# Performance work log

Hardware: AMD Instinct MI355X
Metric: run time of the kernel (lower is better)

## Reference

```python
import jax, jax.numpy as jnp
import numpy as np
import math

NUM_HEADS = 12
EMBED_DIM = 768

def setup_inputs() -> dict:
    key = jax.random.key(0)
    ks = jax.random.split(key, 9)
    B, T, D = 2, 2048, EMBED_DIM
    s = 1.0 / math.sqrt(D)
    inp = {
        "x": jax.random.normal(ks[0], (B, T, D), dtype=jnp.float32),
        "Wq": jax.random.normal(ks[1], (D, D), dtype=jnp.float32) * s,
        "bq": jnp.zeros((D,), dtype=jnp.float32),
        "Wk": jax.random.normal(ks[2], (D, D), dtype=jnp.float32) * s,
        "bk": jnp.zeros((D,), dtype=jnp.float32),
        "Wv": jax.random.normal(ks[3], (D, D), dtype=jnp.float32) * s,
        "bv": jnp.zeros((D,), dtype=jnp.float32),
        "Wo": jax.random.normal(ks[4], (D, D), dtype=jnp.float32) * s,
        "bo": jnp.zeros((D,), dtype=jnp.float32),
    }
    return inp

def reference(x, Wq, bq, Wk, bk, Wv, bv, Wo, bo):
    B, T, D = x.shape
    H = NUM_HEADS
    Dh = D // H
    # QKV projections, split heads: [B, H, T, Dh]
    def proj(W, b):
        y = x @ W.T + b
        return y.reshape(B, T, H, Dh).transpose(0, 2, 1, 3)
    q = proj(Wq, bq)
    k = proj(Wk, bk)
    v = proj(Wv, bv)
    scores = jnp.einsum('bhtd,bhsd->bhts', q, k) / math.sqrt(Dh)  # [B,H,T,T]
    attn = jax.nn.softmax(scores, axis=-1)
    ctx = jnp.einsum('bhts,bhsd->bhtd', attn, v)  # [B,H,T,Dh]
    ctx = ctx.transpose(0, 2, 1, 3).reshape(B, T, D)
    out = ctx @ Wo.T + bo
    return out
```

## Files before the change

### kernel.cpp

```cpp
#include <hip/hip_runtime.h>
#include <math.h>

using f32x4   = __attribute__((ext_vector_type(4))) float;
using bf16x8  = __attribute__((ext_vector_type(8))) short;

constexpr int Bb = 2;
constexpr int T  = 2048;
constexpr int D  = 768;
constexpr int H  = 12;
constexpr int Dh = 64;
constexpr int M  = Bb * T;
constexpr int NQKV = 3 * D;
constexpr int NBH = Bb * H;
#define SCALE_Q 0.18033688011112042f

__device__ __forceinline__ unsigned short f2bf(float f) {
    unsigned u = __float_as_uint(f);
    u += 0x7fffu + ((u >> 16) & 1u);
    return (unsigned short)(u >> 16);
}

__device__ __forceinline__ ushort4 f2bf4(float4 f) {
    return make_ushort4(f2bf(f.x), f2bf(f.y), f2bf(f.z), f2bf(f.w));
}

__device__ __forceinline__ unsigned permpk(float hi_f, float lo_f) {
    return __builtin_amdgcn_perm(__float_as_uint(hi_f), __float_as_uint(lo_f),
                                 0x07060302u);
}

__device__ __forceinline__ void async_copy16(const void* g, void* lds_base) {
    __builtin_amdgcn_global_load_lds(
        (const __attribute__((address_space(1))) unsigned int*)g,
        (__attribute__((address_space(3))) unsigned int*)lds_base, 16, 0, 0);
}

__global__ __launch_bounds__(256) void prep_kernel(
    const float4* __restrict__ x,
    const float4* __restrict__ Wq, const float4* __restrict__ Wk,
    const float4* __restrict__ Wv, const float4* __restrict__ Wo,
    const float* __restrict__ bq, const float* __restrict__ bk, const float* __restrict__ bv,
    ushort4* __restrict__ Xb, ushort4* __restrict__ Wqkvb, ushort4* __restrict__ Wob,
    float* __restrict__ biasS)
{
    const int stride = gridDim.x * 256;
    const int i0 = blockIdx.x * 256 + threadIdx.x;
    const int NX = M * D / 4;
    const int NW = D * D / 4;
    for (int i = i0; i < NX; i += stride) Xb[i] = f2bf4(x[i]);
    for (int i = i0; i < NW; i += stride) {
        Wqkvb[i]          = f2bf4(Wq[i]);
        Wqkvb[NW + i]     = f2bf4(Wk[i]);
        Wqkvb[2 * NW + i] = f2bf4(Wv[i]);
        Wob[i]            = f2bf4(Wo[i]);
    }
    for (int i = i0; i < D; i += stride) {
        biasS[i]         = bq[i];
        biasS[D + i]     = bk[i];
        biasS[2 * D + i] = bv[i];
    }
}

template <int MODE, int TM, int DB>
__global__ __launch_bounds__(256) void gemm_bt_kernel(
    const unsigned short* __restrict__ A, const unsigned short* __restrict__ Bm,
    const float* __restrict__ bias, const int Kdim, const int Ndim,
    float* __restrict__ Cout,
    unsigned short* __restrict__ Qo, unsigned short* __restrict__ Ko,
    unsigned short* __restrict__ Vo)
{
    constexpr int IW  = TM / 32;
    constexpr int NCH = (TM + 128) / 8;
    constexpr int TB  = (TM + 128) * 128;
    __shared__ unsigned short Sm[(TM + 128) * 64 * (DB ? 2 : 1)];
    const int tid  = threadIdx.x;
    const int lane = tid & 63, wv = tid >> 6;
    const int l15  = lane & 15, l4 = lane >> 4;
    const int wr   = wv >> 1,  wc = wv & 1;

    const int lin = blockIdx.y * gridDim.x + blockIdx.x;
    const int gx  = (lin >> 3) % gridDim.x;
    const int gy  = (lin / (8 * gridDim.x)) * 8 + (lin & 7);
    const int row0 = gy * TM, col0 = gx * 128;

    auto stage = [&](int k0, int b) {
        #pragma unroll
        for (int ch0 = 0; ch0 < NCH; ch0 += 4) {
            const int ch = ch0 + wv;
            const int offb = ch * 1024;
            const int off  = offb + lane * 16;
            const int r  = off >> 7;
            const int bl = (off & 127) >> 4;
            const int gc = (bl ^ (r & 7)) << 3;
            const unsigned short* src = (r < TM)
                ? A  + (size_t)(row0 + r) * Kdim + k0 + gc
                : Bm + (size_t)(col0 + (r - TM)) * Kdim + k0 + gc;
            async_copy16(src, (char*)Sm + b * TB + offb);
        }
    };

    f32x4 acc[IW][4];
    #pragma unroll
    for (int i = 0; i < IW; ++i)
        #pragma unroll
        for (int j = 0; j < 4; ++j)
            acc[i][j] = (f32x4){0.f, 0.f, 0.f, 0.f};

    if (DB) stage(0, 0);

    for (int k0 = 0, it = 0; k0 < Kdim; k0 += 64, ++it) {
        const int cur = DB ? (it & 1) : 0;
        __syncthreads();
        if (DB) {
            if (k0 + 64 < Kdim) stage(k0 + 64, cur ^ 1);
        } else {
            stage(k0, 0);
            __syncthreads();
        }
        const char* Sb_ = (const char*)Sm + cur * TB;

        #pragma unroll
        for (int c = 0; c < 2; ++c) {
            bf16x8 af[IW], bfr[4];
            #pragma unroll
            for (int i = 0; i < IW; ++i) {
                const int row = wr * (TM / 2) + i * 16 + l15;
                af[i] = *(const bf16x8*)(Sb_ +
                        row * 128 + (((c << 2) + l4) ^ (row & 7)) * 16);
            }
            #pragma unroll
            for (int j = 0; j < 4; ++j) {
                const int row = TM + wc * 64 + j * 16 + l15;
                bfr[j] = *(const bf16x8*)(Sb_ +
                        row * 128 + (((c << 2) + l4) ^ (row & 7)) * 16);
            }
            #pragma unroll
            for (int i = 0; i < IW; ++i)
                #pragma unroll
                for (int j = 0; j < 4; ++j)
                    acc[i][j] = __builtin_amdgcn_mfma_f32_16x16x32_bf16(af[i], bfr[j], acc[i][j], 0, 0, 0);
        }
    }

    if (MODE == 0) {
        #pragma unroll
        for (int j = 0; j < 4; ++j) {
            const int n = col0 + wc * 64 + j * 16 + l15;
            const float bv_ = bias[n];
            #pragma unroll
            for (int i = 0; i < IW; ++i) {
                #pragma unroll
                for (int r = 0; r < 4; ++r) {
                    const int m = row0 + wr * (TM / 2) + i * 16 + l4 * 4 + r;
                    Cout[(size_t)m * Ndim + n] = acc[i][j][r] + bv_;
                }
            }
        }
    } else {
        #pragma unroll
        for (int j = 0; j < 4; ++j) {
            const int n = col0 + wc * 64 + j * 16 + l15;
            const int which = n / D;
            const int hd = n % D;
            const int h = hd >> 6, d = hd & 63;
            const float bv_ = bias[n];
            if (which == 2) {
                #pragma unroll
                for (int i = 0; i < IW; ++i) {
                    const int m0 = row0 + wr * (TM / 2) + i * 16 + l4 * 4;
                    const int b = m0 >> 11, t = m0 & (T - 1);
                    const int g = (t >> 2) & 3, h16 = (t >> 4) & 1;
                    const int tp = (t & ~31) | (g << 3) | (h16 << 2);
                    float4 v4;
                    v4.x = acc[i][j][0] + bv_; v4.y = acc[i][j][1] + bv_;
                    v4.z = acc[i][j][2] + bv_; v4.w = acc[i][j][3] + bv_;
                    *(ushort4*)&Vo[((size_t)(b * H + h) * Dh + d) * T + tp] = f2bf4(v4);
                }
            } else {
                const float scale = (which == 0) ? SCALE_Q : 1.0f;
                unsigned short* dst = (which == 0) ? Qo : Ko;
                #pragma unroll
                for (int i = 0; i < IW; ++i) {
                    #pragma unroll
                    for (int r = 0; r < 4; ++r) {
                        const int m = row0 + wr * (TM / 2) + i * 16 + l4 * 4 + r;
                        const int b = m >> 11, t = m & (T - 1);
                        dst[((size_t)(b * H + h) * T + t) * Dh + d] =
                            f2bf((acc[i][j][r] + bv_) * scale);
                    }
                }
            }
        }
    }
}

__global__ __launch_bounds__(256) void attn_kernel(
    const unsigned short* __restrict__ Q, const unsigned short* __restrict__ Kg,
    const unsigned short* __restrict__ Vt,
    float* __restrict__ Po, float* __restrict__ PoL)
{
    __shared__ unsigned short Ks[2][64 * 64];
    __shared__ unsigned short Vs[2][64 * 64];
    const int bh = blockIdx.y;
    const int half = blockIdx.z;
    const int q0 = blockIdx.x * 128;
    const int tid = threadIdx.x, lane = tid & 63, wv = tid >> 6;
    const int l15 = lane & 15, l4 = lane >> 4;
    const unsigned short* Qp = Q  + (size_t)bh * T * Dh;
    const unsigned short* Kp = Kg + (size_t)bh * T * Dh;
    const unsigned short* Vp = Vt + (size_t)bh * Dh * T;

    bf16x8 qf[2][2];
    #pragma unroll
    for (int qg = 0; qg < 2; ++qg)
        #pragma unroll
        for (int c = 0; c < 2; ++c)
            qf[qg][c] = *(const bf16x8*)&Qp[(size_t)(q0 + wv * 32 + qg * 16 + l15) * Dh + c * 32 + l4 * 8];

    const short oneb = (short)0x3F80;
    const bf16x8 onesf = {oneb, oneb, oneb, oneb, oneb, oneb, oneb, oneb};

    auto load_tiles = [&](int kt, int buf) {
        #pragma unroll
        for (int i = 0; i < 2; ++i) {
            const int offb = wv * 2048 + i * 1024;
            const int off  = offb + lane * 16;
            const int r = off >> 7;
            const int blk = (off & 127) >> 4;
            const int gc = (blk ^ (r & 7)) << 3;
            async_copy16(Kp + (size_t)(kt + r) * Dh + gc, (char*)&Ks[buf][0] + offb);
            async_copy16(Vp + (size_t)r * T + kt + gc,    (char*)&Vs[buf][0] + offb);
        }
    };

    const int NT = T / 128;
    const int kt0 = half * NT;
    load_tiles(kt0 * 64, 0);
    f32x4 o[2][4], oL[2];
    #pragma unroll
    for (int qg = 0; qg < 2; ++qg) {
        #pragma unroll
        for (int nj = 0; nj < 4; ++nj) o[qg][nj] = (f32x4){0.f, 0.f, 0.f, 0.f};
        oL[qg] = (f32x4){0.f, 0.f, 0.f, 0.f};
    }

    for (int it = 0; it < NT; ++it) {
        const int kt64 = kt0 + it;
        const int cur = it & 1;
        __syncthreads();
        if (it + 1 < NT) load_tiles((kt64 + 1) * 64, cur ^ 1);

        const char* Kb = (const char*)&Ks[cur][0];
        const char* Vb = (const char*)&Vs[cur][0];

        f32x4 Sa[2][2];
        #pragma unroll
        for (int t = 0; t < 2; ++t)
            #pragma unroll
            for (int qg = 0; qg < 2; ++qg)
                Sa[t][qg] = (f32x4){0.f, 0.f, 0.f, 0.f};
        #pragma unroll
        for (int c = 0; c < 2; ++c) {
            #pragma unroll
            for (int t = 0; t < 2; ++t) {
                const int row = t * 16 + l15;
                bf16x8 kb = *(const bf16x8*)(Kb + row * 128 + (((c << 2) + l4) ^ (row & 7)) * 16);
                #pragma unroll
                for (int qg = 0; qg < 2; ++qg)
                    Sa[t][qg] = __builtin_amdgcn_mfma_f32_16x16x32_bf16(kb, qf[qg][c], Sa[t][qg], 0, 0, 0);
            }
        }
        #pragma unroll
        for (int t = 0; t < 2; ++t)
            #pragma unroll
            for (int qg = 0; qg < 2; ++qg)
                #pragma unroll
                for (int r = 0; r < 4; ++r)
                    Sa[t][qg][r] = __builtin_amdgcn_exp2f(Sa[t][qg][r]);
        union { unsigned u[4]; bf16x8 v; } p0[2];
        #pragma unroll
        for (int qg = 0; qg < 2; ++qg) {
            p0[qg].u[0] = permpk(Sa[0][qg][1], Sa[0][qg][0]);
            p0[qg].u[1] = permpk(Sa[0][qg][3], Sa[0][qg][2]);
            p0[qg].u[2] = permpk(Sa[1][qg][1], Sa[1][qg][0]);
            p0[qg].u[3] = permpk(Sa[1][qg][3], Sa[1][qg][2]);
        }

        f32x4 Sb[2][2];
        #pragma unroll
        for (int t = 0; t < 2; ++t)
            #pragma unroll
            for (int qg = 0; qg < 2; ++qg)
                Sb[t][qg] = (f32x4){0.f, 0.f, 0.f, 0.f};
        #pragma unroll
        for (int c = 0; c < 2; ++c) {
            #pragma unroll
            for (int t = 0; t < 2; ++t) {
                const int row = (t + 2) * 16 + l15;
                bf16x8 kb = *(const bf16x8*)(Kb + row * 128 + (((c << 2) + l4) ^ (row & 7)) * 16);
                #pragma unroll
                for (int qg = 0; qg < 2; ++qg)
                    Sb[t][qg] = __builtin_amdgcn_mfma_f32_16x16x32_bf16(kb, qf[qg][c], Sb[t][qg], 0, 0, 0);
            }
        }

        #pragma unroll
        for (int qg = 0; qg < 2; ++qg)
            oL[qg] = __builtin_amdgcn_mfma_f32_16x16x32_bf16(p0[qg].v, onesf, oL[qg], 0, 0, 0);
        #pragma unroll
        for (int nj = 0; nj < 4; ++nj) {
            const int row = nj * 16 + l15;
            bf16x8 vb = *(const bf16x8*)(Vb + row * 128 + ((l4) ^ (row & 7)) * 16);
            #pragma unroll
            for (int qg = 0; qg < 2; ++qg)
                o[qg][nj] = __builtin_amdgcn_mfma_f32_16x16x32_bf16(p0[qg].v, vb, o[qg][nj], 0, 0, 0);
        }

        #pragma unroll
        for (int t = 0; t < 2; ++t)
            #pragma unroll
            for (int qg = 0; qg < 2; ++qg)
                #pragma unroll
                for (int r = 0; r < 4; ++r)
                    Sb[t][qg][r] = __builtin_amdgcn_exp2f(Sb[t][qg][r]);
        union { unsigned u[4]; bf16x8 v; } p1[2];
        #pragma unroll
        for (int qg = 0; qg < 2; ++qg) {
            p1[qg].u[0] = permpk(Sb[0][qg][1], Sb[0][qg][0]);
            p1[qg].u[1] = permpk(Sb[0][qg][3], Sb[0][qg][2]);
            p1[qg].u[2] = permpk(Sb[1][qg][1], Sb[1][qg][0]);
            p1[qg].u[3] = permpk(Sb[1][qg][3], Sb[1][qg][2]);
        }

        #pragma unroll
        for (int qg = 0; qg < 2; ++qg)
            oL[qg] = __builtin_amdgcn_mfma_f32_16x16x32_bf16(p1[qg].v, onesf, oL[qg], 0, 0, 0);
        #pragma unroll
        for (int nj = 0; nj < 4; ++nj) {
            const int row = nj * 16 + l15;
            bf16x8 vb = *(const bf16x8*)(Vb + row * 128 + ((4 + l4) ^ (row & 7)) * 16);
            #pragma unroll
            for (int qg = 0; qg < 2; ++qg)
                o[qg][nj] = __builtin_amdgcn_mfma_f32_16x16x32_bf16(p1[qg].v, vb, o[qg][nj], 0, 0, 0);
        }
    }

    const size_t base = (size_t)(half * NBH + bh) * T;
    #pragma unroll
    for (int qg = 0; qg < 2; ++qg) {
        #pragma unroll
        for (int r = 0; r < 4; ++r) {
            const int t = q0 + wv * 32 + qg * 16 + l4 * 4 + r;
            #pragma unroll
            for (int nj = 0; nj < 4; ++nj)
                Po[(base + t) * 64 + nj * 16 + l15] = o[qg][nj][r];
            if (l15 == 0) PoL[base + t] = oL[qg][r];
        }
    }
}

__global__ __launch_bounds__(256) void combine_kernel(
    const float4* __restrict__ Po, const float* __restrict__ PoL,
    unsigned short* __restrict__ Ctx)
{
    const int idx = blockIdx.x * 256 + threadIdx.x;
    const int d4 = idx & 15;
    const int rem = idx >> 4;
    const int t = rem & (T - 1), bh = rem >> 11;
    const float4 a = Po[(size_t)rem * 16 + d4];
    const float4 c = Po[(size_t)NBH * T * 16 + (size_t)rem * 16 + d4];
    const float inv = 1.0f / (PoL[rem] + PoL[NBH * T + rem]);
    const int b = bh / H, h = bh % H;
    float4 v;
    v.x = (a.x + c.x) * inv; v.y = (a.y + c.y) * inv;
    v.z = (a.z + c.z) * inv; v.w = (a.w + c.w) * inv;
    *(ushort4*)&Ctx[(size_t)(b * T + t) * D + h * 64 + d4 * 4] = f2bf4(v);
}

extern "C" void kernel_launch(void* const* d_in, const int* in_sizes, int n_in,
                              void* d_out, int out_size, void* d_ws, size_t ws_size,
                              hipStream_t stream) {
    const float* x  = (const float*)d_in[0];
    const float* Wq = (const float*)d_in[1];
    const float* bq = (const float*)d_in[2];
    const float* Wk = (const float*)d_in[3];
    const float* bk = (const float*)d_in[4];
    const float* Wv = (const float*)d_in[5];
    const float* bv = (const float*)d_in[6];
    const float* Wo = (const float*)d_in[7];
    const float* bo = (const float*)d_in[8];
    float* out = (float*)d_out;

    char* w = (char*)d_ws;
    auto alloc = [&](size_t bytes) {
        char* p = w; w += (bytes + 255) & ~(size_t)255; return p;
    };
    unsigned short* Xb    = (unsigned short*)alloc((size_t)M * D * 2);
    unsigned short* Wqkvb = (unsigned short*)alloc((size_t)NQKV * D * 2);
    unsigned short* Wob   = (unsigned short*)alloc((size_t)D * D * 2);
    float*          biasS = (float*)alloc((size_t)NQKV * 4);
    unsigned short* Qb    = (unsigned short*)alloc((size_t)M * D * 2);
    unsigned short* Kb    = (unsigned short*)alloc((size_t)M * D * 2);
    unsigned short* Vtb   = (unsigned short*)alloc((size_t)M * D * 2);
    unsigned short* Ctxb  = (unsigned short*)alloc((size_t)M * D * 2);
    float*          Po    = (float*)alloc((size_t)2 * NBH * T * 64 * 4);
    float*          PoL   = (float*)alloc((size_t)2 * NBH * T * 4);

    prep_kernel<<<2048, 256, 0, stream>>>(
        (const float4*)x, (const float4*)Wq, (const float4*)Wk, (const float4*)Wv,
        (const float4*)Wo, bq, bk, bv,
        (ushort4*)Xb, (ushort4*)Wqkvb, (ushort4*)Wob, biasS);

    gemm_bt_kernel<1, 128, 0><<<dim3(NQKV / 128, M / 128), 256, 0, stream>>>(
        Xb, Wqkvb, biasS, D, NQKV, nullptr, Qb, Kb, Vtb);

    attn_kernel<<<dim3(T / 128, NBH, 2), 256, 0, stream>>>(Qb, Kb, Vtb, Po, PoL);

    combine_kernel<<<NBH * T * 16 / 256, 256, 0, stream>>>(
        (const float4*)Po, PoL, Ctxb);

    gemm_bt_kernel<0, 32, 1><<<dim3(D / 128, M / 32), 256, 0, stream>>>(
        Ctxb, Wob, bo, D, D, out, nullptr, nullptr, nullptr);
}
```

Before: 160.9 us.

## Fuse split-KV combine into output projection GEMM A-tile staging

The attention kernel now writes its two partial outputs as bf16 directly in the [B,T,D] context layout, and the separate combine kernel is removed. The output-projection GEMM (new MODE 3) loads both partial tiles through registers, sums them, normalises by the summed row denominators, converts to bf16 and writes the result into shared memory, while B tiles still use async copies. This removes one launch and the fp32 partial-output round trip through global memory. In exchange the A-tile loads go through registers with extra per-tile work, and the unnormalised partials are rounded to bf16 before the sum, which costs some precision.

```diff
diff --git a/kernel.cpp b/kernel.cpp
--- a/kernel.cpp
+++ b/kernel.cpp
@@ -67,7 +67,7 @@
     const float* __restrict__ bias, const int Kdim, const int Ndim,
     float* __restrict__ Cout,
     unsigned short* __restrict__ Qo, unsigned short* __restrict__ Ko,
-    unsigned short* __restrict__ Vo)
+    unsigned short* __restrict__ Vo, const float* __restrict__ PoLp)
 {
     constexpr int IW  = TM / 32;
     constexpr int NCH = (TM + 128) / 8;
@@ -99,6 +99,45 @@
         }
     };
 
+    const int a_offb = wv * 1024;
+    const int a_off  = a_offb + lane * 16;
+    const int a_r    = a_off >> 7;
+    const int a_gc   = (((a_off & 127) >> 4) ^ (a_r & 7)) << 3;
+    const int a_m    = row0 + a_r;
+    const int a_b    = a_m >> 11, a_t = a_m & (T - 1);
+    bf16x8 ar0, ar1; float al0, al1;
+    auto issueA = [&](int k0) {
+        const unsigned short* s0 = A + (size_t)a_m * Kdim + k0 + a_gc;
+        ar0 = *(const bf16x8*)s0;
+        ar1 = *(const bf16x8*)(s0 + (size_t)M * Kdim);
+        const int bhh = a_b * H + (k0 >> 6);
+        al0 = PoLp[(size_t)bhh * T + a_t];
+        al1 = PoLp[(size_t)(NBH + bhh) * T + a_t];
+    };
+    auto writeA = [&](int b) {
+        const float inv = 1.0f / (al0 + al1);
+        union { unsigned short us[8]; bf16x8 v; } cr;
+        #pragma unroll
+        for (int j = 0; j < 8; ++j) {
+            const float f0 = __uint_as_float(((unsigned)(unsigned short)ar0[j]) << 16);
+            const float f1 = __uint_as_float(((unsigned)(unsigned short)ar1[j]) << 16);
+            cr.us[j] = f2bf((f0 + f1) * inv);
+        }
+        *(bf16x8*)((char*)Sm + b * TB + a_off) = cr.v;
+    };
+    auto stageB = [&](int k0, int b) {
+        #pragma unroll
+        for (int ch0 = 0; ch0 < 16; ch0 += 4) {
+            const int ch = (TM / 8) + ch0 + wv;
+            const int offb = ch * 1024;
+            const int off  = offb + lane * 16;
+            const int r  = off >> 7;
+            const int gc = ((((off & 127) >> 4)) ^ (r & 7)) << 3;
+            async_copy16(Bm + (size_t)(col0 + (r - TM)) * Kdim + k0 + gc,
+                         (char*)Sm + b * TB + offb);
+        }
+    };
+
     f32x4 acc[IW][4];
     #pragma unroll
     for (int i = 0; i < IW; ++i)
@@ -106,13 +145,20 @@
         for (int j = 0; j < 4; ++j)
             acc[i][j] = (f32x4){0.f, 0.f, 0.f, 0.f};
 
-    if (DB) stage(0, 0);
+    if (DB) {
+        if constexpr (MODE == 3) { issueA(0); stageB(0, 0); writeA(0); }
+        else stage(0, 0);
+    }
 
     for (int k0 = 0, it = 0; k0 < Kdim; k0 += 64, ++it) {
         const int cur = DB ? (it & 1) : 0;
         __syncthreads();
+        const bool more = (k0 + 64 < Kdim);
         if (DB) {
-            if (k0 + 64 < Kdim) stage(k0 + 64, cur ^ 1);
+            if (more) {
+                if constexpr (MODE == 3) { issueA(k0 + 64); stageB(k0 + 64, cur ^ 1); }
+                else stage(k0 + 64, cur ^ 1);
+            }
         } else {
             stage(k0, 0);
             __syncthreads();
@@ -140,9 +186,11 @@
                 for (int j = 0; j < 4; ++j)
                     acc[i][j] = __builtin_amdgcn_mfma_f32_16x16x32_bf16(af[i], bfr[j], acc[i][j], 0, 0, 0);
         }
-    }
-
-    if (MODE == 0) {
+
+        if constexpr (MODE == 3) { if (more) writeA(cur ^ 1); }
+    }
+
+    if (MODE == 0 || MODE == 3) {
         #pragma unroll
         for (int j = 0; j < 4; ++j) {
             const int n = col0 + wc * 64 + j * 16 + l15;
@@ -197,7 +245,7 @@
 __global__ __launch_bounds__(256) void attn_kernel(
     const unsigned short* __restrict__ Q, const unsigned short* __restrict__ Kg,
     const unsigned short* __restrict__ Vt,
-    float* __restrict__ Po, float* __restrict__ PoL)
+    unsigned short* __restrict__ Pb, float* __restrict__ PoL)
 {
     __shared__ unsigned short Ks[2][64 * 64];
     __shared__ unsigned short Vs[2][64 * 64];
@@ -345,7 +393,8 @@
         }
     }
 
-    const size_t base = (size_t)(half * NBH + bh) * T;
+    const int b = bh / H, h = bh % H;
+    unsigned short* Pw = Pb + (size_t)half * M * D;
     #pragma unroll
     for (int qg = 0; qg < 2; ++qg) {
         #pragma unroll
@@ -353,28 +402,10 @@
             const int t = q0 + wv * 32 + qg * 16 + l4 * 4 + r;
             #pragma unroll
             for (int nj = 0; nj < 4; ++nj)
-                Po[(base + t) * 64 + nj * 16 + l15] = o[qg][nj][r];
-            if (l15 == 0) PoL[base + t] = oL[qg][r];
-        }
-    }
-}
-
-__global__ __launch_bounds__(256) void combine_kernel(
-    const float4* __restrict__ Po, const float* __restrict__ PoL,
-    unsigned short* __restrict__ Ctx)
-{
-    const int idx = blockIdx.x * 256 + threadIdx.x;
-    const int d4 = idx & 15;
-    const int rem = idx >> 4;
-    const int t = rem & (T - 1), bh = rem >> 11;
-    const float4 a = Po[(size_t)rem * 16 + d4];
-    const float4 c = Po[(size_t)NBH * T * 16 + (size_t)rem * 16 + d4];
-    const float inv = 1.0f / (PoL[rem] + PoL[NBH * T + rem]);
-    const int b = bh / H, h = bh % H;
-    float4 v;
-    v.x = (a.x + c.x) * inv; v.y = (a.y + c.y) * inv;
-    v.z = (a.z + c.z) * inv; v.w = (a.w + c.w) * inv;
-    *(ushort4*)&Ctx[(size_t)(b * T + t) * D + h * 64 + d4 * 4] = f2bf4(v);
+                Pw[(size_t)(b * T + t) * D + h * 64 + nj * 16 + l15] = f2bf(o[qg][nj][r]);
+            if (l15 == 0) PoL[(size_t)(half * NBH + bh) * T + t] = oL[qg][r];
+        }
+    }
 }
 
 extern "C" void kernel_launch(void* const* d_in, const int* in_sizes, int n_in,
@@ -402,8 +433,7 @@
     unsigned short* Qb    = (unsigned short*)alloc((size_t)M * D * 2);
     unsigned short* Kb    = (unsigned short*)alloc((size_t)M * D * 2);
     unsigned short* Vtb   = (unsigned short*)alloc((size_t)M * D * 2);
-    unsigned short* Ctxb  = (unsigned short*)alloc((size_t)M * D * 2);
-    float*          Po    = (float*)alloc((size_t)2 * NBH * T * 64 * 4);
+    unsigned short* Pb    = (unsigned short*)alloc((size_t)2 * M * D * 2);
     float*          PoL   = (float*)alloc((size_t)2 * NBH * T * 4);
 
     prep_kernel<<<2048, 256, 0, stream>>>(
@@ -412,13 +442,10 @@
         (ushort4*)Xb, (ushort4*)Wqkvb, (ushort4*)Wob, biasS);
 
     gemm_bt_kernel<1, 128, 0><<<dim3(NQKV / 128, M / 128), 256, 0, stream>>>(
-        Xb, Wqkvb, biasS, D, NQKV, nullptr, Qb, Kb, Vtb);
-
-    attn_kernel<<<dim3(T / 128, NBH, 2), 256, 0, stream>>>(Qb, Kb, Vtb, Po, PoL);
-
-    combine_kernel<<<NBH * T * 16 / 256, 256, 0, stream>>>(
-        (const float4*)Po, PoL, Ctxb);
-
-    gemm_bt_kernel<0, 32, 1><<<dim3(D / 128, M / 32), 256, 0, stream>>>(
-        Ctxb, Wob, bo, D, D, out, nullptr, nullptr, nullptr);
-}
+        Xb, Wqkvb, biasS, D, NQKV, nullptr, Qb, Kb, Vtb, nullptr);
+
+    attn_kernel<<<dim3(T / 128, NBH, 2), 256, 0, stream>>>(Qb, Kb, Vtb, Pb, PoL);
+
+    gemm_bt_kernel<3, 32, 1><<<dim3(D / 128, M / 32), 256, 0, stream>>>(
+        Pb, Wob, bo, D, D, out, nullptr, nullptr, nullptr, PoL);
+}
```

Measured after the change: 155.3 us. 1.04x faster.
